# Optimization experiments

Hardware: AMD Instinct MI355X
Metric: run time of the kernel (lower is better)

## Reference

```python
import jax, jax.numpy as jnp
import numpy as np

N_ATOMS = 300000
N_COLS = 8
VOCAB = 4096      # nn.Embedding(4096, per_col_dim)
D_COL = 32        # per_col_dim
HID = 256         # hidden_size
N_BONDS = 320000
B_GRAPHS = 6000
ATOMS_PER_GRAPH = 50
STEPS = 3
SENTINEL = 999999999


def _linear_params(key, fan_in, fan_out):
    lim = 1.0 / np.sqrt(fan_in)
    kw, kb = jax.random.split(key)
    W = jax.random.uniform(kw, (fan_out, fan_in), minval=-lim, maxval=lim, dtype=jnp.float32)
    b = jax.random.uniform(kb, (fan_out,), minval=-lim, maxval=lim, dtype=jnp.float32)
    return W, b


def setup_inputs() -> dict:
    key = jax.random.key(0)
    ks = jax.random.split(key, 8)
    a_features = jax.random.randint(ks[0], (N_ATOMS, N_COLS), 0, VOCAB, dtype=jnp.int32)
    uv = jax.random.randint(ks[1], (N_BONDS, 2), 0, N_ATOMS, dtype=jnp.int32)
    bextra = jax.random.randint(ks[2], (N_BONDS, 1), 0, 16, dtype=jnp.int32)
    b_features = jnp.concatenate([uv, bextra], axis=1)
    # contiguous equal-length scopes: graph i owns atoms [i*50, i*50+50)
    starts = np.arange(B_GRAPHS, dtype=np.int32) * ATOMS_PER_GRAPH
    lengths = np.full(B_GRAPHS, ATOMS_PER_GRAPH, dtype=np.int32)
    a_scopes = jnp.asarray(np.stack([starts, lengths], axis=1))
    emb_weights = jax.random.normal(ks[3], (N_COLS, VOCAB, D_COL), dtype=jnp.float32) * 0.02
    W_in, b_in = _linear_params(ks[4], D_COL, HID)
    W_self, b_self = _linear_params(ks[5], HID, HID)
    W_neigh, b_neigh = _linear_params(ks[6], HID, HID)
    W_out, b_out = _linear_params(ks[7], HID, HID)
    return {
        'a_features': a_features, 'b_features': b_features, 'a_scopes': a_scopes,
        'emb_weights': emb_weights,
        'W_in': W_in, 'b_in': b_in,
        'W_self': W_self, 'b_self': b_self,
        'W_neigh': W_neigh, 'b_neigh': b_neigh,
        'W_out': W_out, 'b_out': b_out,
    }


def reference(a_features, b_features, a_scopes, emb_weights,
              W_in, b_in, W_self, b_self, W_neigh, b_neigh, W_out, b_out):
    # --- per-column embedding lookup, summed over columns ---
    idx = jnp.remainder(a_features, VOCAB)
    idx = jnp.where(a_features >= SENTINEL, 0, idx)          # sentinel -> index 0
    x = jnp.zeros((a_features.shape[0], D_COL), dtype=emb_weights.dtype)
    for c in range(N_COLS):                                   # fixed small loop over columns
        x = x + emb_weights[c][idx[:, c]]
    h = x @ W_in.T + b_in                                     # [N, HID]
    # --- undirected edges -> two directed edge lists ---
    u = b_features[:, 0]
    v = b_features[:, 1]
    src = jnp.concatenate([u, v], axis=0)
    dst = jnp.concatenate([v, u], axis=0)
    # --- message passing steps ---
    for _ in range(STEPS):
        agg = jnp.zeros_like(h).at[dst].add(h[src])           # scatter-add neighbor sum
        h = jax.nn.relu(h @ W_self.T + b_self + agg @ W_neigh.T + b_neigh)
    h = h @ W_out.T + b_out
    # --- per-graph mean pooling over contiguous scopes ---
    lengths = a_scopes[:, 1]
    seg_ids = jnp.repeat(jnp.arange(a_scopes.shape[0]), lengths,
                         total_repeat_length=h.shape[0])
    sums = jax.ops.segment_sum(h, seg_ids, num_segments=a_scopes.shape[0])
    denom = jnp.maximum(lengths, 1).astype(h.dtype)[:, None]
    return sums / denom
```

## Files before the change

### kernel.cpp

```cpp
#include <hip/hip_runtime.h>

#define NATOMS 300000
#define NCOLS 8
#define VOCABSZ 4096
#define DCOL 32
#define HIDDIM 256
#define NBONDS 320000
#define NGRAPHS 6000
#define NSTEPS 3

constexpr int MP = 300032;
constexpr int MTILES64 = MP / 64;

typedef _Float16 f16;
typedef _Float16 f16x4 __attribute__((ext_vector_type(4)));
typedef _Float16 f16x8 __attribute__((ext_vector_type(8)));
typedef float f32x4 __attribute__((ext_vector_type(4)));

constexpr float LO_SCALE = 2048.0f;
constexpr float INV_LO   = 1.0f / 2048.0f;

__device__ __forceinline__ void split2(float x, f16& h, f16& l) {
    h = (f16)x;
    l = (f16)((x - (float)h) * LO_SCALE);
}

__device__ __forceinline__ int swz(int row, int q) {
    return (row * 4 + (q ^ ((row >> 1) & 3))) * 8;
}

static void* g_pool = nullptr;
__attribute__((constructor)) static void alloc_pool() {
    void* p = nullptr;
    if (hipMalloc(&p, (size_t)1024 * 1024 * 1024) == hipSuccess) {
        hipMemset(p, 0, (size_t)1024 * 1024 * 1024);
        g_pool = p;
    }
}

__global__ void fill_kernel(float* out, float v, int n) {
    int i = blockIdx.x * blockDim.x + threadIdx.x;
    if (i < n) out[i] = v;
}

__global__ void build_edges_kernel(const int* __restrict__ bf, int* __restrict__ esrc,
                                   int* __restrict__ nxt, int* head) {
    int e = blockIdx.x * blockDim.x + threadIdx.x;
    if (e >= 2 * NBONDS) return;
    int src, dst;
    if (e < NBONDS) { src = bf[e * 3 + 0]; dst = bf[e * 3 + 1]; }
    else { int i = e - NBONDS; src = bf[i * 3 + 1]; dst = bf[i * 3 + 0]; }
    esrc[e] = src;
    nxt[e] = atomicExch(&head[dst], e);
}

__global__ void wsplit_kernel(const float* __restrict__ W, f16* __restrict__ Wh,
                              f16* __restrict__ Wl, int n) {
    int i = blockIdx.x * blockDim.x + threadIdx.x;
    if (i >= n) return;
    split2(W[i], Wh[i], Wl[i]);
}

__global__ void bsum_kernel(const float* __restrict__ a, const float* __restrict__ b,
                            float* __restrict__ o) {
    int i = threadIdx.x;
    o[i] = a[i] + b[i];
}

__global__ void embed_kernel(const int* __restrict__ af, const float* __restrict__ emb,
                             f16* __restrict__ xh, f16* __restrict__ xl) {
    int gid = blockIdx.x * blockDim.x + threadIdx.x;
    int i = gid >> 5, k = gid & 31;
    if (i >= NATOMS) return;
    float s = 0.0f;
#pragma unroll
    for (int c = 0; c < NCOLS; c++) {
        int v = af[i * NCOLS + c];
        int idx = v & (VOCABSZ - 1);
        if (v >= 999999999) idx = 0;
        s += emb[((size_t)c * VOCABSZ + idx) * DCOL + k];
    }
    split2(s, xh[(size_t)i * DCOL + k], xl[(size_t)i * DCOL + k]);
}

__global__ void agg_kernel(const f16* __restrict__ Ahi, const f16* __restrict__ Alo,
                           f16* __restrict__ Ghi, f16* __restrict__ Glo,
                           const int* __restrict__ head, const int* __restrict__ nxt,
                           const int* __restrict__ esrc) {
    int wid = (blockIdx.x * blockDim.x + threadIdx.x) >> 6;
    int lane = threadIdx.x & 63;
    if (wid >= NATOMS) return;
    float4 sh = make_float4(0.f, 0.f, 0.f, 0.f);
    float4 sl = make_float4(0.f, 0.f, 0.f, 0.f);
    int e = head[wid];
    while (e >= 0) {
        int src = esrc[e];
        const f16x4 vh = *(const f16x4*)(Ahi + (size_t)src * HIDDIM + lane * 4);
        const f16x4 vl = *(const f16x4*)(Alo + (size_t)src * HIDDIM + lane * 4);
        sh.x += (float)vh.x; sh.y += (float)vh.y; sh.z += (float)vh.z; sh.w += (float)vh.w;
        sl.x += (float)vl.x; sl.y += (float)vl.y; sl.z += (float)vl.z; sl.w += (float)vl.w;
        e = nxt[e];
    }
    float4 s;
    s.x = sh.x + sl.x * INV_LO; s.y = sh.y + sl.y * INV_LO;
    s.z = sh.z + sl.z * INV_LO; s.w = sh.w + sl.w * INV_LO;
    f16 h0, l0, h1, l1, h2, l2, h3, l3;
    split2(s.x, h0, l0); split2(s.y, h1, l1);
    split2(s.z, h2, l2); split2(s.w, h3, l3);
    f16x4 oh, ol;
    oh.x = h0; oh.y = h1; oh.z = h2; oh.w = h3;
    ol.x = l0; ol.y = l1; ol.z = l2; ol.w = l3;
    *(f16x4*)(Ghi + (size_t)wid * HIDDIM + lane * 4) = oh;
    *(f16x4*)(Glo + (size_t)wid * HIDDIM + lane * 4) = ol;
}

template <bool HAS_A2, bool RELU, int K>
__global__ __launch_bounds__(256, 2) void mfma_gemm(
    const f16* __restrict__ A1h, const f16* __restrict__ A1l,
    const f16* __restrict__ A2h, const f16* __restrict__ A2l,
    const f16* __restrict__ B1h, const f16* __restrict__ B1l,
    const f16* __restrict__ B2h, const f16* __restrict__ B2l,
    const float* __restrict__ bias,
    f16* __restrict__ Chi, f16* __restrict__ Clo) {
    __shared__ __align__(16) f16 sAh[64 * 32];
    __shared__ __align__(16) f16 sAl[64 * 32];
    __shared__ __align__(16) f16 sBh[256 * 32];
    __shared__ __align__(16) f16 sBl[256 * 32];

    const int t = threadIdx.x;
    const int m0 = blockIdx.x * 64;
    const int lane = t & 63;
    const int wid = t >> 6;
    const int wn = wid * 64;
    const int quad = lane >> 4;
    const int l16 = lane & 15;
    const int ra = t >> 2;
    const int qa = t & 3;

    f32x4 acch[4][4], accl[4][4];
#pragma unroll
    for (int a = 0; a < 4; a++)
#pragma unroll
        for (int b = 0; b < 4; b++) {
            acch[a][b] = (f32x4){0.f, 0.f, 0.f, 0.f};
            accl[a][b] = (f32x4){0.f, 0.f, 0.f, 0.f};
        }

    constexpr int NMAT = HAS_A2 ? 2 : 1;
    constexpr int NST = (K / 32) * NMAT;

    int4 pAh, pAl, pBh0, pBh1, pBh2, pBh3, pBl0, pBl1, pBl2, pBl3;

#define LOAD_STAGE(S)                                                          \
    {                                                                          \
        const int mat_ = HAS_A2 ? ((S) & 1) : 0;                               \
        const int kb_ = (HAS_A2 ? ((S) >> 1) : (S)) * 32;                      \
        const f16* Ah_ = (mat_ == 0) ? A1h : A2h;                              \
        const f16* Al_ = (mat_ == 0) ? A1l : A2l;                              \
        const f16* Bh_ = (mat_ == 0) ? B1h : B2h;                              \
        const f16* Bl_ = (mat_ == 0) ? B1l : B2l;                              \
        const size_t ao_ = (size_t)(m0 + ra) * K + kb_ + qa * 8;               \
        pAh = *(const int4*)(Ah_ + ao_);                                       \
        pAl = *(const int4*)(Al_ + ao_);                                       \
        const size_t bo_ = (size_t)ra * K + kb_ + qa * 8;                      \
        pBh0 = *(const int4*)(Bh_ + bo_);                                      \
        pBh1 = *(const int4*)(Bh_ + bo_ + (size_t)64 * K);                     \
        pBh2 = *(const int4*)(Bh_ + bo_ + (size_t)128 * K);                    \
        pBh3 = *(const int4*)(Bh_ + bo_ + (size_t)192 * K);                    \
        pBl0 = *(const int4*)(Bl_ + bo_);                                      \
        pBl1 = *(const int4*)(Bl_ + bo_ + (size_t)64 * K);                     \
        pBl2 = *(const int4*)(Bl_ + bo_ + (size_t)128 * K);                    \
        pBl3 = *(const int4*)(Bl_ + bo_ + (size_t)192 * K);                    \
    }

    LOAD_STAGE(0);

    for (int s = 0; s < NST; s++) {
        __syncthreads();
        {
            const int dA = swz(ra, qa);
            *(int4*)(sAh + dA) = pAh;
            *(int4*)(sAl + dA) = pAl;
            const int d0 = swz(ra, qa), d1 = swz(ra + 64, qa);
            const int d2 = swz(ra + 128, qa), d3 = swz(ra + 192, qa);
            *(int4*)(sBh + d0) = pBh0; *(int4*)(sBh + d1) = pBh1;
            *(int4*)(sBh + d2) = pBh2; *(int4*)(sBh + d3) = pBh3;
            *(int4*)(sBl + d0) = pBl0; *(int4*)(sBl + d1) = pBl1;
            *(int4*)(sBl + d2) = pBl2; *(int4*)(sBl + d3) = pBl3;
        }
        __syncthreads();
        if (s + 1 < NST) LOAD_STAGE(s + 1);

        f16x8 fah[4], fal[4];
#pragma unroll
        for (int mt = 0; mt < 4; mt++) {
            const int src = swz(mt * 16 + l16, quad);
            fah[mt] = *(const f16x8*)(sAh + src);
            fal[mt] = *(const f16x8*)(sAl + src);
        }
#pragma unroll
        for (int nt = 0; nt < 4; nt++) {
            const int src = swz(wn + nt * 16 + l16, quad);
            const f16x8 bh = *(const f16x8*)(sBh + src);
            const f16x8 bl = *(const f16x8*)(sBl + src);
#pragma unroll
            for (int mt = 0; mt < 4; mt++) {
                acch[mt][nt] = __builtin_amdgcn_mfma_f32_16x16x32_f16(fah[mt], bh, acch[mt][nt], 0, 0, 0);
                accl[mt][nt] = __builtin_amdgcn_mfma_f32_16x16x32_f16(fah[mt], bl, accl[mt][nt], 0, 0, 0);
                accl[mt][nt] = __builtin_amdgcn_mfma_f32_16x16x32_f16(fal[mt], bh, accl[mt][nt], 0, 0, 0);
            }
        }
    }
#undef LOAD_STAGE

#pragma unroll
    for (int mt = 0; mt < 4; mt++) {
#pragma unroll
        for (int nt = 0; nt < 4; nt++) {
            const int col = wn + nt * 16 + l16;
            const float bv = bias[col];
#pragma unroll
            for (int r = 0; r < 4; r++) {
                const int row = m0 + mt * 16 + quad * 4 + r;
                float v = acch[mt][nt][r] + accl[mt][nt][r] * INV_LO + bv;
                if (RELU) v = fmaxf(v, 0.f);
                f16 hi, lo;
                split2(v, hi, lo);
                Chi[(size_t)row * HIDDIM + col] = hi;
                Clo[(size_t)row * HIDDIM + col] = lo;
            }
        }
    }
}

__global__ void readout_mean_kernel(const f16* __restrict__ Hhi, const f16* __restrict__ Hlo,
                                    const int* __restrict__ scopes, float* __restrict__ G) {
    int g = blockIdx.x;
    int n = threadIdx.x;
    int start = scopes[g * 2 + 0];
    int len = scopes[g * 2 + 1];
    float s = 0.f;
    for (int j = 0; j < len; j++) {
        size_t o = (size_t)(start + j) * HIDDIM + n;
        s += (float)Hhi[o] + (float)Hlo[o] * INV_LO;
    }
    int d = len > 1 ? len : 1;
    G[(size_t)g * HIDDIM + n] = s / (float)d;
}

__global__ __launch_bounds__(256) void out_gemm_kernel(
    const float* __restrict__ G, const float* __restrict__ W,
    const float* __restrict__ bias, float* __restrict__ out) {
    __shared__ float sG[16 * 256];
    const int g0 = blockIdx.x * 16;
    const int t = threadIdx.x;
#pragma unroll
    for (int i = 0; i < 16; i++) sG[i * 256 + t] = G[(size_t)(g0 + i) * 256 + t];
    __syncthreads();
    const float bv = bias[t];
    const float* wrow = W + (size_t)t * 256;
    float acc[16];
#pragma unroll
    for (int g = 0; g < 16; g++) acc[g] = 0.f;
    for (int k = 0; k < 256; k += 4) {
        const float4 w = *(const float4*)(wrow + k);
#pragma unroll
        for (int g = 0; g < 16; g++) {
            const float4 a = *(const float4*)(sG + g * 256 + k);
            acc[g] = fmaf(a.x, w.x, acc[g]);
            acc[g] = fmaf(a.y, w.y, acc[g]);
            acc[g] = fmaf(a.z, w.z, acc[g]);
            acc[g] = fmaf(a.w, w.w, acc[g]);
        }
    }
#pragma unroll
    for (int g = 0; g < 16; g++) out[(size_t)(g0 + g) * 256 + t] = acc[g] + bv;
}

extern "C" void kernel_launch(void* const* d_in, const int* in_sizes, int n_in,
                              void* d_out, int out_size, void* d_ws, size_t ws_size,
                              hipStream_t stream) {
    const int* a_features = (const int*)d_in[0];
    const int* b_features = (const int*)d_in[1];
    const int* a_scopes   = (const int*)d_in[2];
    const float* emb      = (const float*)d_in[3];
    const float* W_in     = (const float*)d_in[4];
    const float* b_in     = (const float*)d_in[5];
    const float* W_self   = (const float*)d_in[6];
    const float* b_self   = (const float*)d_in[7];
    const float* W_neigh  = (const float*)d_in[8];
    const float* b_neigh  = (const float*)d_in[9];
    const float* W_out    = (const float*)d_in[10];
    const float* b_out    = (const float*)d_in[11];

    if (g_pool == nullptr) {
        fill_kernel<<<(out_size + 255) / 256, 256, 0, stream>>>(
            (float*)d_out, 77777.0f, out_size);
        return;
    }

    f16* p = (f16*)g_pool;
    const size_t HB = (size_t)MP * HIDDIM;
    f16* hAhi = p;            f16* hAlo = p + HB;
    f16* hBhi = p + 2 * HB;   f16* hBlo = p + 3 * HB;
    f16* hChi = p + 4 * HB;   f16* hClo = p + 5 * HB;
    f16* xhi  = p + 6 * HB;
    f16* xlo  = xhi + (size_t)MP * DCOL;
    f16* Winh = xlo + (size_t)MP * DCOL;
    f16* Winl = Winh + HIDDIM * DCOL;
    f16* Wsh  = Winl + HIDDIM * DCOL;
    f16* Wsl  = Wsh + HIDDIM * HIDDIM;
    f16* Wnh  = Wsl + HIDDIM * HIDDIM;
    f16* Wnl  = Wnh + HIDDIM * HIDDIM;
    float* Gmean = (float*)(Wnl + HIDDIM * HIDDIM);
    float* bsum  = Gmean + (size_t)NGRAPHS * HIDDIM;
    int* esrc = (int*)(bsum + HIDDIM);
    int* nxt  = esrc + 2 * NBONDS;
    int* head = nxt + 2 * NBONDS;

    constexpr int NPAD = MP - NATOMS;

    hipMemsetAsync(head, 0xFF, (size_t)MP * sizeof(int), stream);
    build_edges_kernel<<<(2 * NBONDS + 255) / 256, 256, 0, stream>>>(b_features, esrc, nxt, head);
    wsplit_kernel<<<(HIDDIM * DCOL + 255) / 256, 256, 0, stream>>>(W_in, Winh, Winl, HIDDIM * DCOL);
    wsplit_kernel<<<(HIDDIM * HIDDIM + 255) / 256, 256, 0, stream>>>(W_self, Wsh, Wsl, HIDDIM * HIDDIM);
    wsplit_kernel<<<(HIDDIM * HIDDIM + 255) / 256, 256, 0, stream>>>(W_neigh, Wnh, Wnl, HIDDIM * HIDDIM);
    bsum_kernel<<<1, HIDDIM, 0, stream>>>(b_self, b_neigh, bsum);

    constexpr int PADF = NPAD * HIDDIM / 2;
    fill_kernel<<<(PADF + 255) / 256, 256, 0, stream>>>((float*)(hAhi + (size_t)NATOMS * HIDDIM), 0.f, PADF);
    fill_kernel<<<(PADF + 255) / 256, 256, 0, stream>>>((float*)(hAlo + (size_t)NATOMS * HIDDIM), 0.f, PADF);
    fill_kernel<<<(PADF + 255) / 256, 256, 0, stream>>>((float*)(hBhi + (size_t)NATOMS * HIDDIM), 0.f, PADF);
    fill_kernel<<<(PADF + 255) / 256, 256, 0, stream>>>((float*)(hBlo + (size_t)NATOMS * HIDDIM), 0.f, PADF);
    fill_kernel<<<(PADF + 255) / 256, 256, 0, stream>>>((float*)(hChi + (size_t)NATOMS * HIDDIM), 0.f, PADF);
    fill_kernel<<<(PADF + 255) / 256, 256, 0, stream>>>((float*)(hClo + (size_t)NATOMS * HIDDIM), 0.f, PADF);
    constexpr int PADX = NPAD * DCOL / 2;
    fill_kernel<<<(PADX + 255) / 256, 256, 0, stream>>>((float*)(xhi + (size_t)NATOMS * DCOL), 0.f, PADX);
    fill_kernel<<<(PADX + 255) / 256, 256, 0, stream>>>((float*)(xlo + (size_t)NATOMS * DCOL), 0.f, PADX);

    embed_kernel<<<(NATOMS * DCOL + 255) / 256, 256, 0, stream>>>(a_features, emb, xhi, xlo);
    mfma_gemm<false, false, DCOL><<<MTILES64, 256, 0, stream>>>(
        xhi, xlo, nullptr, nullptr, Winh, Winl, nullptr, nullptr, b_in, hAhi, hAlo);

    f16 *h_hi = hAhi, *h_lo = hAlo;
    f16 *g_hi = hBhi, *g_lo = hBlo;
    f16 *n_hi = hChi, *n_lo = hClo;
    for (int s = 0; s < NSTEPS; s++) {
        agg_kernel<<<NATOMS / 4, 256, 0, stream>>>(h_hi, h_lo, g_hi, g_lo, head, nxt, esrc);
        mfma_gemm<true, true, HIDDIM><<<MTILES64, 256, 0, stream>>>(
            h_hi, h_lo, g_hi, g_lo, Wsh, Wsl, Wnh, Wnl, bsum, n_hi, n_lo);
        f16* t1 = h_hi; f16* t2 = h_lo;
        h_hi = n_hi; h_lo = n_lo;
        n_hi = g_hi; n_lo = g_lo;
        g_hi = t1;   g_lo = t2;
    }

    readout_mean_kernel<<<NGRAPHS, 256, 0, stream>>>(h_hi, h_lo, a_scopes, Gmean);
    out_gemm_kernel<<<NGRAPHS / 16, 256, 0, stream>>>(Gmean, W_out, b_out, (float*)d_out);
}
```

Baseline: 2.042 ms.

## Merge hi/lo MFMA accumulators, rescale split-fp16 weights, raise GEMM occupancy

The split-fp16 GEMM now accumulates the hi*hi, hi*lo and lo*hi products into a single fp32 accumulator instead of two. To keep the low-part products in fp16 range, the weights are pre-scaled by 128 and the residuals are stored unscaled. This halves the accumulator registers, which lets the launch bounds ask for 3 blocks per CU instead of 2. The register-staged prefetch of the next K-slice is removed, so global loads are no longer overlapped with the MFMAs. Storing unscaled activation residuals risks fp16 subnormal precision loss for small values.

After: 2.653 ms. +29.9%, slower.

```diff
diff --git a/kernel.cpp b/kernel.cpp
--- a/kernel.cpp
+++ b/kernel.cpp
@@ -17,12 +17,12 @@
 typedef _Float16 f16x8 __attribute__((ext_vector_type(8)));
 typedef float f32x4 __attribute__((ext_vector_type(4)));
 
-constexpr float LO_SCALE = 2048.0f;
-constexpr float INV_LO   = 1.0f / 2048.0f;
+constexpr float W_SCALE = 128.0f;
+constexpr float INV_W   = 1.0f / 128.0f;
 
 __device__ __forceinline__ void split2(float x, f16& h, f16& l) {
     h = (f16)x;
-    l = (f16)((x - (float)h) * LO_SCALE);
+    l = (f16)(x - (float)h);
 }
 
 __device__ __forceinline__ int swz(int row, int q) {
@@ -58,7 +58,7 @@
                               f16* __restrict__ Wl, int n) {
     int i = blockIdx.x * blockDim.x + threadIdx.x;
     if (i >= n) return;
-    split2(W[i], Wh[i], Wl[i]);
+    split2(W[i] * W_SCALE, Wh[i], Wl[i]);
 }
 
 __global__ void bsum_kernel(const float* __restrict__ a, const float* __restrict__ b,
@@ -102,8 +102,8 @@
         e = nxt[e];
     }
     float4 s;
-    s.x = sh.x + sl.x * INV_LO; s.y = sh.y + sl.y * INV_LO;
-    s.z = sh.z + sl.z * INV_LO; s.w = sh.w + sl.w * INV_LO;
+    s.x = sh.x + sl.x; s.y = sh.y + sl.y;
+    s.z = sh.z + sl.z; s.w = sh.w + sl.w;
     f16 h0, l0, h1, l1, h2, l2, h3, l3;
     split2(s.x, h0, l0); split2(s.y, h1, l1);
     split2(s.z, h2, l2); split2(s.w, h3, l3);
@@ -115,7 +115,7 @@
 }
 
 template <bool HAS_A2, bool RELU, int K>
-__global__ __launch_bounds__(256, 2) void mfma_gemm(
+__global__ __launch_bounds__(256, 3) void mfma_gemm(
     const f16* __restrict__ A1h, const f16* __restrict__ A1l,
     const f16* __restrict__ A2h, const f16* __restrict__ A2l,
     const f16* __restrict__ B1h, const f16* __restrict__ B1l,
@@ -137,81 +137,58 @@
     const int ra = t >> 2;
     const int qa = t & 3;
 
-    f32x4 acch[4][4], accl[4][4];
+    f32x4 acc[4][4];
 #pragma unroll
     for (int a = 0; a < 4; a++)
 #pragma unroll
-        for (int b = 0; b < 4; b++) {
-            acch[a][b] = (f32x4){0.f, 0.f, 0.f, 0.f};
-            accl[a][b] = (f32x4){0.f, 0.f, 0.f, 0.f};
+        for (int b = 0; b < 4; b++) acc[a][b] = (f32x4){0.f, 0.f, 0.f, 0.f};
+
+    const int NMAT = HAS_A2 ? 2 : 1;
+    for (int kb = 0; kb < K; kb += 32) {
+        for (int mat = 0; mat < NMAT; mat++) {
+            const f16* Ah = (mat == 0) ? A1h : A2h;
+            const f16* Al = (mat == 0) ? A1l : A2l;
+            const f16* Bh = (mat == 0) ? B1h : B2h;
+            const f16* Bl = (mat == 0) ? B1l : B2l;
+            __syncthreads();
+            {
+                const int dst = swz(ra & 63, qa);
+                const size_t ao = (size_t)(m0 + (ra & 63)) * K + kb + qa * 8;
+                *(int4*)(sAh + dst) = *(const int4*)(Ah + ao);
+                *(int4*)(sAl + dst) = *(const int4*)(Al + ao);
+            }
+#pragma unroll
+            for (int i = 0; i < 4; i++) {
+                const int u = t + 256 * i;
+                const int r = u >> 2, q = u & 3;
+                const int dst = swz(r, q);
+                const size_t bo = (size_t)r * K + kb + q * 8;
+                *(int4*)(sBh + dst) = *(const int4*)(Bh + bo);
+                *(int4*)(sBl + dst) = *(const int4*)(Bl + bo);
+            }
+            __syncthreads();
+
+            f16x8 fah[4], fal[4];
+#pragma unroll
+            for (int mt = 0; mt < 4; mt++) {
+                const int src = swz(mt * 16 + l16, quad);
+                fah[mt] = *(const f16x8*)(sAh + src);
+                fal[mt] = *(const f16x8*)(sAl + src);
+            }
+#pragma unroll
+            for (int nt = 0; nt < 4; nt++) {
+                const int src = swz(wn + nt * 16 + l16, quad);
+                const f16x8 bh = *(const f16x8*)(sBh + src);
+                const f16x8 bl = *(const f16x8*)(sBl + src);
+#pragma unroll
+                for (int mt = 0; mt < 4; mt++) {
+                    acc[mt][nt] = __builtin_amdgcn_mfma_f32_16x16x32_f16(fah[mt], bh, acc[mt][nt], 0, 0, 0);
+                    acc[mt][nt] = __builtin_amdgcn_mfma_f32_16x16x32_f16(fah[mt], bl, acc[mt][nt], 0, 0, 0);
+                    acc[mt][nt] = __builtin_amdgcn_mfma_f32_16x16x32_f16(fal[mt], bh, acc[mt][nt], 0, 0, 0);
+                }
+            }
         }
-
-    constexpr int NMAT = HAS_A2 ? 2 : 1;
-    constexpr int NST = (K / 32) * NMAT;
-
-    int4 pAh, pAl, pBh0, pBh1, pBh2, pBh3, pBl0, pBl1, pBl2, pBl3;
-
-#define LOAD_STAGE(S)                                                          \
-    {                                                                          \
-        const int mat_ = HAS_A2 ? ((S) & 1) : 0;                               \
-        const int kb_ = (HAS_A2 ? ((S) >> 1) : (S)) * 32;                      \
-        const f16* Ah_ = (mat_ == 0) ? A1h : A2h;                              \
-        const f16* Al_ = (mat_ == 0) ? A1l : A2l;                              \
-        const f16* Bh_ = (mat_ == 0) ? B1h : B2h;                              \
-        const f16* Bl_ = (mat_ == 0) ? B1l : B2l;                              \
-        const size_t ao_ = (size_t)(m0 + ra) * K + kb_ + qa * 8;               \
-        pAh = *(const int4*)(Ah_ + ao_);                                       \
-        pAl = *(const int4*)(Al_ + ao_);                                       \
-        const size_t bo_ = (size_t)ra * K + kb_ + qa * 8;                      \
-        pBh0 = *(const int4*)(Bh_ + bo_);                                      \
-        pBh1 = *(const int4*)(Bh_ + bo_ + (size_t)64 * K);                     \
-        pBh2 = *(const int4*)(Bh_ + bo_ + (size_t)128 * K);                    \
-        pBh3 = *(const int4*)(Bh_ + bo_ + (size_t)192 * K);                    \
-        pBl0 = *(const int4*)(Bl_ + bo_);                                      \
-        pBl1 = *(const int4*)(Bl_ + bo_ + (size_t)64 * K);                     \
-        pBl2 = *(const int4*)(Bl_ + bo_ + (size_t)128 * K);                    \
-        pBl3 = *(const int4*)(Bl_ + bo_ + (size_t)192 * K);                    \
-    }
-
-    LOAD_STAGE(0);
-
-    for (int s = 0; s < NST; s++) {
-        __syncthreads();
-        {
-            const int dA = swz(ra, qa);
-            *(int4*)(sAh + dA) = pAh;
-            *(int4*)(sAl + dA) = pAl;
-            const int d0 = swz(ra, qa), d1 = swz(ra + 64, qa);
-            const int d2 = swz(ra + 128, qa), d3 = swz(ra + 192, qa);
-            *(int4*)(sBh + d0) = pBh0; *(int4*)(sBh + d1) = pBh1;
-            *(int4*)(sBh + d2) = pBh2; *(int4*)(sBh + d3) = pBh3;
-            *(int4*)(sBl + d0) = pBl0; *(int4*)(sBl + d1) = pBl1;
-            *(int4*)(sBl + d2) = pBl2; *(int4*)(sBl + d3) = pBl3;
-        }
-        __syncthreads();
-        if (s + 1 < NST) LOAD_STAGE(s + 1);
-
-        f16x8 fah[4], fal[4];
-#pragma unroll
-        for (int mt = 0; mt < 4; mt++) {
-            const int src = swz(mt * 16 + l16, quad);
-            fah[mt] = *(const f16x8*)(sAh + src);
-            fal[mt] = *(const f16x8*)(sAl + src);
-        }
-#pragma unroll
-        for (int nt = 0; nt < 4; nt++) {
-            const int src = swz(wn + nt * 16 + l16, quad);
-            const f16x8 bh = *(const f16x8*)(sBh + src);
-            const f16x8 bl = *(const f16x8*)(sBl + src);
-#pragma unroll
-            for (int mt = 0; mt < 4; mt++) {
-                acch[mt][nt] = __builtin_amdgcn_mfma_f32_16x16x32_f16(fah[mt], bh, acch[mt][nt], 0, 0, 0);
-                accl[mt][nt] = __builtin_amdgcn_mfma_f32_16x16x32_f16(fah[mt], bl, accl[mt][nt], 0, 0, 0);
-                accl[mt][nt] = __builtin_amdgcn_mfma_f32_16x16x32_f16(fal[mt], bh, accl[mt][nt], 0, 0, 0);
-            }
-        }
-    }
-#undef LOAD_STAGE
+    }
 
 #pragma unroll
     for (int mt = 0; mt < 4; mt++) {
@@ -222,7 +199,7 @@
 #pragma unroll
             for (int r = 0; r < 4; r++) {
                 const int row = m0 + mt * 16 + quad * 4 + r;
-                float v = acch[mt][nt][r] + accl[mt][nt][r] * INV_LO + bv;
+                float v = acc[mt][nt][r] * INV_W + bv;
                 if (RELU) v = fmaxf(v, 0.f);
                 f16 hi, lo;
                 split2(v, hi, lo);
@@ -242,7 +219,7 @@
     float s = 0.f;
     for (int j = 0; j < len; j++) {
         size_t o = (size_t)(start + j) * HIDDIM + n;
-        s += (float)Hhi[o] + (float)Hlo[o] * INV_LO;
+        s += (float)Hhi[o] + (float)Hlo[o];
     }
     int d = len > 1 ? len : 1;
     G[(size_t)g * HIDDIM + n] = s / (float)d;
```

## Interleave hi/lo f16 halves per row for activations and aggregation

Applied to the files above, without the earlier changes.

Stores each activation row as [hi(256) | lo(256)] in one buffer instead of separate hi and lo arrays. The gather in the aggregation kernel then issues one 16-byte load per lane covering both halves, which touches fewer scattered cache lines, and the hi/lo partial sums are combined with a cross-half shuffle. The GEMM, embed and readout kernels are updated to the new strided layout. Per-row stores in the GEMM epilogue now go to two regions of the same row.

Result: no change. 2.010 ms (-1.6%).

```diff
diff --git a/kernel.cpp b/kernel.cpp
--- a/kernel.cpp
+++ b/kernel.cpp
@@ -11,9 +11,10 @@
 
 constexpr int MP = 300032;
 constexpr int MTILES64 = MP / 64;
+constexpr int HSTR = 2 * HIDDIM;
+constexpr int XSTR = 2 * DCOL;
 
 typedef _Float16 f16;
-typedef _Float16 f16x4 __attribute__((ext_vector_type(4)));
 typedef _Float16 f16x8 __attribute__((ext_vector_type(8)));
 typedef float f32x4 __attribute__((ext_vector_type(4)));
 
@@ -68,7 +69,7 @@
 }
 
 __global__ void embed_kernel(const int* __restrict__ af, const float* __restrict__ emb,
-                             f16* __restrict__ xh, f16* __restrict__ xl) {
+                             f16* __restrict__ x) {
     int gid = blockIdx.x * blockDim.x + threadIdx.x;
     int i = gid >> 5, k = gid & 31;
     if (i >= NATOMS) return;
@@ -80,48 +81,59 @@
         if (v >= 999999999) idx = 0;
         s += emb[((size_t)c * VOCABSZ + idx) * DCOL + k];
     }
-    split2(s, xh[(size_t)i * DCOL + k], xl[(size_t)i * DCOL + k]);
-}
-
-__global__ void agg_kernel(const f16* __restrict__ Ahi, const f16* __restrict__ Alo,
-                           f16* __restrict__ Ghi, f16* __restrict__ Glo,
+    f16 hi, lo;
+    split2(s, hi, lo);
+    x[(size_t)i * XSTR + k] = hi;
+    x[(size_t)i * XSTR + DCOL + k] = lo;
+}
+
+__global__ void agg_kernel(const f16* __restrict__ H, f16* __restrict__ G,
                            const int* __restrict__ head, const int* __restrict__ nxt,
                            const int* __restrict__ esrc) {
     int wid = (blockIdx.x * blockDim.x + threadIdx.x) >> 6;
     int lane = threadIdx.x & 63;
     if (wid >= NATOMS) return;
-    float4 sh = make_float4(0.f, 0.f, 0.f, 0.f);
-    float4 sl = make_float4(0.f, 0.f, 0.f, 0.f);
+    float a0 = 0.f, a1 = 0.f, a2 = 0.f, a3 = 0.f,
+          a4 = 0.f, a5 = 0.f, a6 = 0.f, a7 = 0.f;
     int e = head[wid];
     while (e >= 0) {
         int src = esrc[e];
-        const f16x4 vh = *(const f16x4*)(Ahi + (size_t)src * HIDDIM + lane * 4);
-        const f16x4 vl = *(const f16x4*)(Alo + (size_t)src * HIDDIM + lane * 4);
-        sh.x += (float)vh.x; sh.y += (float)vh.y; sh.z += (float)vh.z; sh.w += (float)vh.w;
-        sl.x += (float)vl.x; sl.y += (float)vl.y; sl.z += (float)vl.z; sl.w += (float)vl.w;
+        const f16x8 v = *(const f16x8*)(H + (size_t)src * HSTR + lane * 8);
+        a0 += (float)v[0]; a1 += (float)v[1]; a2 += (float)v[2]; a3 += (float)v[3];
+        a4 += (float)v[4]; a5 += (float)v[5]; a6 += (float)v[6]; a7 += (float)v[7];
         e = nxt[e];
     }
-    float4 s;
-    s.x = sh.x + sl.x * INV_LO; s.y = sh.y + sl.y * INV_LO;
-    s.z = sh.z + sl.z * INV_LO; s.w = sh.w + sl.w * INV_LO;
-    f16 h0, l0, h1, l1, h2, l2, h3, l3;
-    split2(s.x, h0, l0); split2(s.y, h1, l1);
-    split2(s.z, h2, l2); split2(s.w, h3, l3);
-    f16x4 oh, ol;
-    oh.x = h0; oh.y = h1; oh.z = h2; oh.w = h3;
-    ol.x = l0; ol.y = l1; ol.z = l2; ol.w = l3;
-    *(f16x4*)(Ghi + (size_t)wid * HIDDIM + lane * 4) = oh;
-    *(f16x4*)(Glo + (size_t)wid * HIDDIM + lane * 4) = ol;
+    const bool isLo = lane >= 32;
+    if (isLo) {
+        a0 *= INV_LO; a1 *= INV_LO; a2 *= INV_LO; a3 *= INV_LO;
+        a4 *= INV_LO; a5 *= INV_LO; a6 *= INV_LO; a7 *= INV_LO;
+    }
+    float s0 = a0 + __shfl_xor(a0, 32, 64);
+    float s1 = a1 + __shfl_xor(a1, 32, 64);
+    float s2 = a2 + __shfl_xor(a2, 32, 64);
+    float s3 = a3 + __shfl_xor(a3, 32, 64);
+    float s4 = a4 + __shfl_xor(a4, 32, 64);
+    float s5 = a5 + __shfl_xor(a5, 32, 64);
+    float s6 = a6 + __shfl_xor(a6, 32, 64);
+    float s7 = a7 + __shfl_xor(a7, 32, 64);
+    f16x8 o;
+#define EMIT(J, S)                                                    \
+    {                                                                 \
+        const f16 hv = (f16)(S);                                      \
+        o[J] = isLo ? (f16)(((S) - (float)hv) * LO_SCALE) : hv;       \
+    }
+    EMIT(0, s0) EMIT(1, s1) EMIT(2, s2) EMIT(3, s3)
+    EMIT(4, s4) EMIT(5, s5) EMIT(6, s6) EMIT(7, s7)
+#undef EMIT
+    *(f16x8*)(G + (size_t)wid * HSTR + lane * 8) = o;
 }
 
 template <bool HAS_A2, bool RELU, int K>
 __global__ __launch_bounds__(256, 2) void mfma_gemm(
-    const f16* __restrict__ A1h, const f16* __restrict__ A1l,
-    const f16* __restrict__ A2h, const f16* __restrict__ A2l,
+    const f16* __restrict__ A1, const f16* __restrict__ A2,
     const f16* __restrict__ B1h, const f16* __restrict__ B1l,
     const f16* __restrict__ B2h, const f16* __restrict__ B2l,
-    const float* __restrict__ bias,
-    f16* __restrict__ Chi, f16* __restrict__ Clo) {
+    const float* __restrict__ bias, f16* __restrict__ C) {
     __shared__ __align__(16) f16 sAh[64 * 32];
     __shared__ __align__(16) f16 sAl[64 * 32];
     __shared__ __align__(16) f16 sBh[256 * 32];
@@ -155,13 +167,12 @@
     {                                                                          \
         const int mat_ = HAS_A2 ? ((S) & 1) : 0;                               \
         const int kb_ = (HAS_A2 ? ((S) >> 1) : (S)) * 32;                      \
-        const f16* Ah_ = (mat_ == 0) ? A1h : A2h;                              \
-        const f16* Al_ = (mat_ == 0) ? A1l : A2l;                              \
+        const f16* A_ = (mat_ == 0) ? A1 : A2;                                 \
         const f16* Bh_ = (mat_ == 0) ? B1h : B2h;                              \
         const f16* Bl_ = (mat_ == 0) ? B1l : B2l;                              \
-        const size_t ao_ = (size_t)(m0 + ra) * K + kb_ + qa * 8;               \
-        pAh = *(const int4*)(Ah_ + ao_);                                       \
-        pAl = *(const int4*)(Al_ + ao_);                                       \
+        const size_t ao_ = (size_t)(m0 + ra) * (2 * K) + kb_ + qa * 8;         \
+        pAh = *(const int4*)(A_ + ao_);                                        \
+        pAl = *(const int4*)(A_ + ao_ + K);                                    \
         const size_t bo_ = (size_t)ra * K + kb_ + qa * 8;                      \
         pBh0 = *(const int4*)(Bh_ + bo_);                                      \
         pBh1 = *(const int4*)(Bh_ + bo_ + (size_t)64 * K);                     \
@@ -226,14 +237,14 @@
                 if (RELU) v = fmaxf(v, 0.f);
                 f16 hi, lo;
                 split2(v, hi, lo);
-                Chi[(size_t)row * HIDDIM + col] = hi;
-                Clo[(size_t)row * HIDDIM + col] = lo;
+                C[(size_t)row * HSTR + col] = hi;
+                C[(size_t)row * HSTR + HIDDIM + col] = lo;
             }
         }
     }
 }
 
-__global__ void readout_mean_kernel(const f16* __restrict__ Hhi, const f16* __restrict__ Hlo,
+__global__ void readout_mean_kernel(const f16* __restrict__ H,
                                     const int* __restrict__ scopes, float* __restrict__ G) {
     int g = blockIdx.x;
     int n = threadIdx.x;
@@ -241,8 +252,8 @@
     int len = scopes[g * 2 + 1];
     float s = 0.f;
     for (int j = 0; j < len; j++) {
-        size_t o = (size_t)(start + j) * HIDDIM + n;
-        s += (float)Hhi[o] + (float)Hlo[o] * INV_LO;
+        const f16* row = H + (size_t)(start + j) * HSTR;
+        s += (float)row[n] + (float)row[HIDDIM + n] * INV_LO;
     }
     int d = len > 1 ? len : 1;
     G[(size_t)g * HIDDIM + n] = s / (float)d;
@@ -300,13 +311,12 @@
     }
 
     f16* p = (f16*)g_pool;
-    const size_t HB = (size_t)MP * HIDDIM;
-    f16* hAhi = p;            f16* hAlo = p + HB;
-    f16* hBhi = p + 2 * HB;   f16* hBlo = p + 3 * HB;
-    f16* hChi = p + 4 * HB;   f16* hClo = p + 5 * HB;
-    f16* xhi  = p + 6 * HB;
-    f16* xlo  = xhi + (size_t)MP * DCOL;
-    f16* Winh = xlo + (size_t)MP * DCOL;
+    const size_t HB2 = (size_t)MP * HSTR;
+    f16* bufA = p;
+    f16* bufB = p + HB2;
+    f16* bufC = p + 2 * HB2;
+    f16* xbuf = p + 3 * HB2;
+    f16* Winh = xbuf + (size_t)MP * XSTR;
     f16* Winl = Winh + HIDDIM * DCOL;
     f16* Wsh  = Winl + HIDDIM * DCOL;
     f16* Wsl  = Wsh + HIDDIM * HIDDIM;
@@ -327,34 +337,28 @@
     wsplit_kernel<<<(HIDDIM * HIDDIM + 255) / 256, 256, 0, stream>>>(W_neigh, Wnh, Wnl, HIDDIM * HIDDIM);
     bsum_kernel<<<1, HIDDIM, 0, stream>>>(b_self, b_neigh, bsum);
 
-    constexpr int PADF = NPAD * HIDDIM / 2;
-    fill_kernel<<<(PADF + 255) / 256, 256, 0, stream>>>((float*)(hAhi + (size_t)NATOMS * HIDDIM), 0.f, PADF);
-    fill_kernel<<<(PADF + 255) / 256, 256, 0, stream>>>((float*)(hAlo + (size_t)NATOMS * HIDDIM), 0.f, PADF);
-    fill_kernel<<<(PADF + 255) / 256, 256, 0, stream>>>((float*)(hBhi + (size_t)NATOMS * HIDDIM), 0.f, PADF);
-    fill_kernel<<<(PADF + 255) / 256, 256, 0, stream>>>((float*)(hBlo + (size_t)NATOMS * HIDDIM), 0.f, PADF);
-    fill_kernel<<<(PADF + 255) / 256, 256, 0, stream>>>((float*)(hChi + (size_t)NATOMS * HIDDIM), 0.f, PADF);
-    fill_kernel<<<(PADF + 255) / 256, 256, 0, stream>>>((float*)(hClo + (size_t)NATOMS * HIDDIM), 0.f, PADF);
-    constexpr int PADX = NPAD * DCOL / 2;
-    fill_kernel<<<(PADX + 255) / 256, 256, 0, stream>>>((float*)(xhi + (size_t)NATOMS * DCOL), 0.f, PADX);
-    fill_kernel<<<(PADX + 255) / 256, 256, 0, stream>>>((float*)(xlo + (size_t)NATOMS * DCOL), 0.f, PADX);
-
-    embed_kernel<<<(NATOMS * DCOL + 255) / 256, 256, 0, stream>>>(a_features, emb, xhi, xlo);
+    constexpr int PADH = NPAD * HSTR / 2;
+    fill_kernel<<<(PADH + 255) / 256, 256, 0, stream>>>((float*)(bufA + (size_t)NATOMS * HSTR), 0.f, PADH);
+    fill_kernel<<<(PADH + 255) / 256, 256, 0, stream>>>((float*)(bufB + (size_t)NATOMS * HSTR), 0.f, PADH);
+    fill_kernel<<<(PADH + 255) / 256, 256, 0, stream>>>((float*)(bufC + (size_t)NATOMS * HSTR), 0.f, PADH);
+    constexpr int PADX = NPAD * XSTR / 2;
+    fill_kernel<<<(PADX + 255) / 256, 256, 0, stream>>>((float*)(xbuf + (size_t)NATOMS * XSTR), 0.f, PADX);
+
+    embed_kernel<<<(NATOMS * DCOL + 255) / 256, 256, 0, stream>>>(a_features, emb, xbuf);
     mfma_gemm<false, false, DCOL><<<MTILES64, 256, 0, stream>>>(
-        xhi, xlo, nullptr, nullptr, Winh, Winl, nullptr, nullptr, b_in, hAhi, hAlo);
-
-    f16 *h_hi = hAhi, *h_lo = hAlo;
-    f16 *g_hi = hBhi, *g_lo = hBlo;
-    f16 *n_hi = hChi, *n_lo = hClo;
+        xbuf, nullptr, Winh, Winl, nullptr, nullptr, b_in, bufA);
+
+    f16* h  = bufA;
+    f16* g  = bufB;
+    f16* hn = bufC;
     for (int s = 0; s < NSTEPS; s++) {
-        agg_kernel<<<NATOMS / 4, 256, 0, stream>>>(h_hi, h_lo, g_hi, g_lo, head, nxt, esrc);
+        agg_kernel<<<NATOMS / 4, 256, 0, stream>>>(h, g, head, nxt, esrc);
         mfma_gemm<true, true, HIDDIM><<<MTILES64, 256, 0, stream>>>(
-            h_hi, h_lo, g_hi, g_lo, Wsh, Wsl, Wnh, Wnl, bsum, n_hi, n_lo);
-        f16* t1 = h_hi; f16* t2 = h_lo;
-        h_hi = n_hi; h_lo = n_lo;
-        n_hi = g_hi; n_lo = g_lo;
-        g_hi = t1;   g_lo = t2;
-    }
-
-    readout_mean_kernel<<<NGRAPHS, 256, 0, stream>>>(h_hi, h_lo, a_scopes, Gmean);
+            h, g, Wsh, Wsl, Wnh, Wnl, bsum, hn);
+        f16* old = h;
+        h = hn; hn = g; g = old;
+    }
+
+    readout_mean_kernel<<<NGRAPHS, 256, 0, stream>>>(h, a_scopes, Gmean);
     out_gemm_kernel<<<NGRAPHS / 16, 256, 0, stream>>>(Gmean, W_out, b_out, (float*)d_out);
 }
```
